# Kernel optimization log

Measured on AMD Instinct MI355X. Metric: run time of the kernel, lower is better.

Reference implementation:

```python
import jax, jax.numpy as jnp
import numpy as np

BS, GS, E, KMAX = 128, 2000, 128, 4
CLIP = 10.0
NEG = -1e30


def _gru(x, hprev, Wih, Whh, bih, bhh):
    # torch.nn.GRUCell math
    gi = x @ Wih.T + bih
    gh = hprev @ Whh.T + bhh
    ir, iz, i_n = jnp.split(gi, 3, axis=-1)
    hr, hz, h_n = jnp.split(gh, 3, axis=-1)
    r = jax.nn.sigmoid(ir + hr)
    z = jax.nn.sigmoid(iz + hz)
    n = jnp.tanh(i_n + r * h_n)
    return (1.0 - z) * n + z * hprev


def setup_inputs() -> dict:
    key = jax.random.key(0)
    it = iter(jax.random.split(key, 40))
    s = 1.0 / float(np.sqrt(E))
    u = lambda shape: jax.random.uniform(next(it), shape, jnp.float32, -s, s)
    inp = {
        "h": jax.random.normal(next(it), (BS, GS, E), jnp.float32),
        "rec": jax.random.randint(next(it), (BS, GS), 0, GS, dtype=jnp.int32),
        "context2": jax.random.normal(next(it), (BS, 9), jnp.float32),
        "visited_time": jax.random.randint(next(it), (BS, GS), 0, GS, dtype=jnp.int32),
        "last_action": jax.random.randint(next(it), (BS, 1), 0, GS, dtype=jnp.int32),
        "fixed_action": jax.random.randint(next(it), (BS, KMAX), 0, GS, dtype=jnp.int32),
    }
    for n in ["W_K1", "W_K2", "W_K3", "W_K4", "W_Q1", "W_Q2", "W_Q3", "W_Q4", "W_init"]:
        inp[n] = u((E, E))
    for n in ["b_init", "V1", "V2", "init_query"]:
        inp[n] = u((E,))
    for r in ["rnn1", "rnn2"]:
        inp[r + "_Wih"] = u((3 * E, E))
        inp[r + "_Whh"] = u((3 * E, E))
        inp[r + "_bih"] = u((3 * E,))
        inp[r + "_bhh"] = u((3 * E,))
    return inp


def _forward(h, rec, visited_time, last_action, fixed_action,
             W_K1, W_K2, W_K3, W_K4, W_Q1, W_Q2, W_Q3, W_Q4, V1, V2,
             W_init, b_init, init_query,
             rnn1_Wih, rnn1_Whh, rnn1_bih, rnn1_bhh,
             rnn2_Wih, rnn2_Whh, rnn2_bih, rnn2_bhh):
    bs, gs, e = h.shape
    cols = jnp.arange(gs)[None, :]          # [1, gs]
    rows = jnp.arange(bs)
    # K projections of h are loop-invariant: hoist them (same math as in-loop recompute)
    K1h = jnp.einsum('bge,fe->bgf', h, W_K1)
    K2h = jnp.einsum('bge,fe->bgf', h, W_K2)
    K3h = jnp.einsum('bge,fe->bgf', h, W_K3)
    K4h = jnp.einsum('bge,fe->bgf', h, W_K4)
    q1 = q2 = h.mean(1) @ W_init.T + b_init
    input_q1 = input_q2 = jnp.broadcast_to(init_query, (bs, e))
    mask = jnp.zeros((bs, gs), bool)
    stopped = jnp.ones((bs,), bool)
    nol = jnp.full((bs, 1), -1, jnp.int32)   # next_of_last_action
    ai = jnp.zeros((bs, KMAX), jnp.int32)    # action_index
    kl = jnp.zeros((bs, KMAX + 1), jnp.int32)
    kr = jnp.zeros((bs, KMAX), jnp.int32)
    ll = jnp.zeros((bs,), h.dtype)
    vtt = None
    for i in range(KMAX):
        q1 = _gru(input_q1, q1, rnn1_Wih, rnn1_Whh, rnn1_bih, rnn1_bhh)
        q2 = _gru(input_q2, q2, rnn2_Wih, rnn2_Whh, rnn2_bih, rnn2_bhh)
        s1 = (V1 * jnp.tanh(K1h + (q1 @ W_Q1.T)[:, None, :] + K3h * (q1 @ W_Q3.T)[:, None, :])).sum(-1)
        s2 = (V2 * jnp.tanh(K2h + (q2 @ W_Q2.T)[:, None, :] + K4h * (q2 @ W_Q4.T)[:, None, :])).sum(-1)
        logits = jnp.tanh(s1 + s2) * CLIP
        logits = jnp.where(mask, NEG, logits)
        if i == 0:
            logits = jnp.where(cols == last_action, NEG, logits)
        action = fixed_action[:, i:i + 1]
        if i > 0:
            action = jnp.where(stopped[:, None], ai[:, 0:1], action)
        logp = jax.nn.log_softmax(logits, axis=-1)
        loss_now = jnp.take_along_axis(logp, action, 1)[:, 0]
        ll = ll + (loss_now if i == 0 else jnp.where(stopped, 0.0, loss_now))
        nna = jnp.take_along_axis(rec, action, 1)  # next_of_new_action [bs,1]
        ai = ai.at[:, i].set(action[:, 0])
        kl = kl.at[:, i].set(jnp.where(stopped, action[:, 0], kl[:, i]))
        kr = kr.at[:, (i - 1) % KMAX].set(jnp.where(stopped, kr[:, (i - 1) % KMAX], action[:, 0]))
        kl = kl.at[:, i + 1].set(nna[:, 0])
        input_q1 = h[rows, action[:, 0]]
        input_q2 = jnp.where(stopped[:, None], input_q1, h[rows, nol[:, 0] % gs])
        eq = (action == nol)[:, 0]
        stopped = eq if i == 0 else (stopped | eq)
        kl = kl.at[:, i].set(jnp.where(stopped, kl[:, (i - 1) % (KMAX + 1)], kl[:, i]))
        kr = kr.at[:, i].set(jnp.where(stopped, kr[:, (i - 1) % KMAX], kr[:, i]))
        if i == 0:
            vtt = (visited_time - jnp.take_along_axis(visited_time, action, 1)) % gs
        vtt_a = jnp.take_along_axis(vtt, action, 1)
        mask = vtt <= vtt_a
        if i == 0:
            mask = mask | (vtt > gs - 2)
        mask = jnp.where(stopped[:, None] & (cols == action), False, mask)
        allow = (~stopped) & (nna[:, 0] == ai[:, 0])
        mask = jnp.where(allow[:, None] & (cols == ai[:, 0:1]), False, mask)
        nol = jnp.where(stopped[:, None], jnp.int32(-1), nna)
    kr = kr.at[:, KMAX - 1].set(jnp.where(~stopped, kl[:, KMAX], kr[:, KMAX - 1]))
    action_all = jnp.concatenate([ai, kl[:, :KMAX], kr], axis=-1)  # [bs, 3*KMAX]
    return action_all, ll


def reference(h, rec, context2, visited_time, last_action, fixed_action,
              W_K1, W_K2, W_K3, W_K4, W_Q1, W_Q2, W_Q3, W_Q4,
              V1, V2, W_init, b_init, init_query,
              rnn1_Wih, rnn1_Whh, rnn1_bih, rnn1_bhh,
              rnn2_Wih, rnn2_Whh, rnn2_bih, rnn2_bhh):
    # context2 unused: with_explore_stat_feature=False path (learned V1/V2)
    return _forward(h, rec, visited_time, last_action, fixed_action,
                    W_K1, W_K2, W_K3, W_K4, W_Q1, W_Q2, W_Q3, W_Q4, V1, V2,
                    W_init, b_init, init_query,
                    rnn1_Wih, rnn1_Whh, rnn1_bih, rnn1_bhh,
                    rnn2_Wih, rnn2_Whh, rnn2_bih, rnn2_bhh)
```

## Files before the change

kernel.cpp:

```cpp
#include <hip/hip_runtime.h>
#include <math.h>

#define BS 128
#define GS 2000
#define E  128
#define KMAXI 4
#define CLIPV 10.0f
#define NEGV  -1.0e30f

typedef __bf16 bf16_t;
typedef __bf16 bf16x8 __attribute__((ext_vector_type(8)));
typedef float fx4 __attribute__((ext_vector_type(4)));
typedef float fx2 __attribute__((ext_vector_type(2)));

__device__ __forceinline__ float fast_sigmoid(float x){ return 1.0f/(1.0f+__expf(-x)); }
__device__ __forceinline__ float fast_tanhf(float x){
    float e = __expf(2.0f*x);
    return 1.0f - 2.0f/(e + 1.0f);
}
__device__ __forceinline__ float pade_tanh(float x){
    float t = __builtin_amdgcn_fmed3f(x, -3.0f, 3.0f);
    float r = t*t;
    float num = t*(27.0f + r);
    float den = fmaf(9.0f, r, 27.0f);
    return num * __builtin_amdgcn_rcpf(den);
}
__device__ __forceinline__ fx2 tanh2_poly(fx2 x){
    fx2 t;
    t.x = __builtin_amdgcn_fmed3f(x.x, -3.0f, 3.0f);
    t.y = __builtin_amdgcn_fmed3f(x.y, -3.0f, 3.0f);
    fx2 r = t*t;
    fx2 q = r*(-0.0015650f) + 0.03172875f;
    q = q*r + (-0.23082094f);
    q = q*r + 0.979947f;
    return t*q;
}
__device__ __forceinline__ int pymod_s(int a){ return a < 0 ? a + GS : a; }

__device__ __forceinline__ void load_lds16(const bf16_t* g, bf16_t* l){
    __builtin_amdgcn_global_load_lds(
        (const __attribute__((address_space(1))) void*)g,
        (__attribute__((address_space(3))) void*)l, 16, 0, 0);
}

#define SC_STRIDE 64

__global__ __launch_bounds__(256) void k_hmean(
    const float* __restrict__ h, float* __restrict__ hpart,
    const int* __restrict__ rec, const int* __restrict__ vtime,
    const int* __restrict__ last_action, const int* __restrict__ fixed_action,
    int* __restrict__ sc, float* __restrict__ out)
{
    int b = blockIdx.x, p = blockIdx.y, tid = threadIdx.x;
    if (p == 16){
        if (b != 0) return;
        int t = tid;
        if (t >= BS) return;
        int stopped = 1, nol = -1;
        int ai[4]={0,0,0,0}, kl[5]={0,0,0,0,0}, kr[4]={0,0,0,0};
        int a0 = 0;
        int* scb = sc + t*SC_STRIDE;
        for (int it=0; it<KMAXI; ++it){
            int action = (it==0) ? fixed_action[t*KMAXI]
                                 : (stopped ? ai[0] : fixed_action[t*KMAXI+it]);
            int old_stopped = stopped;
            if (it==0) a0 = action;
            int vta = (it==0) ? 0 : pymod_s(vtime[(size_t)t*GS+action] - vtime[(size_t)t*GS+a0]);
            int nna = rec[(size_t)t*GS+action];
            int eq  = (action == nol) ? 1 : 0;
            int new_stopped = (it==0) ? eq : (stopped | eq);
            int ai0 = (it==0) ? action : ai[0];
            int allow = (!new_stopped) && (nna == ai0);

            ai[it] = action;
            if (old_stopped)  kl[it] = action;
            if (!old_stopped) kr[(it+3)&3] = action;
            kl[it+1] = nna;
            if (new_stopped) kl[it] = kl[(it+4)%5];
            if (new_stopped) kr[it] = kr[(it+3)&3];

            int row1 = action;
            int i2 = pymod_s(nol);
            int row2 = old_stopped ? row1 : i2;

            int* s_it = scb + 8 + it*8;
            s_it[0]=action; s_it[1]=old_stopped; s_it[2]=new_stopped;
            s_it[3]=allow;  s_it[4]=vta; s_it[5]=row1; s_it[6]=row2;

            nol = new_stopped ? -1 : nna;
            stopped = new_stopped;
        }
        scb[0] = a0;
        if (!stopped) kr[3] = kl[4];
        out[BS*12 + t] = 0.0f;
        for (int j=0;j<4;++j) out[t*12+j]   = (float)ai[j];
        for (int j=0;j<4;++j) out[t*12+4+j] = (float)kl[j];
        for (int j=0;j<4;++j) out[t*12+8+j] = (float)kr[j];
        return;
    }
    int e4 = (tid & 31) * 4;
    int gsub = tid >> 5;
    float4 acc = {0.f,0.f,0.f,0.f};
    int g0 = p*125, g1 = g0+125;
    for (int g = g0 + gsub; g < g1; g += 8){
        float4 v = *(const float4*)(h + ((size_t)b*GS + g)*E + e4);
        acc.x += v.x; acc.y += v.y; acc.z += v.z; acc.w += v.w;
    }
    __shared__ float ps[8][E];
    *(float4*)(&ps[gsub][e4]) = acc;
    __syncthreads();
    if (tid < E){
        float s = 0.f;
        #pragma unroll
        for (int j=0;j<8;++j) s += ps[j][tid];
        hpart[(b*16+p)*E + tid] = s;
    }
}

__device__ __forceinline__ float dot32(const float* a, const float* __restrict__ w){
    const float4* a4=(const float4*)a; const float4* w4=(const float4*)w;
    float s=0.f;
    #pragma unroll 8
    for (int i=0;i<32;++i){ float4 x=a4[i], y=w4[i]; s += x.x*y.x + x.y*y.y + x.z*y.z + x.w*y.w; }
    return s;
}

__global__ __launch_bounds__(384) void k_gru4(
    const float* __restrict__ hpart, const float* __restrict__ W_init,
    const float* __restrict__ b_init, const float* __restrict__ init_query,
    const float* __restrict__ h, const int* __restrict__ sc,
    const float* __restrict__ Wih1, const float* __restrict__ Whh1,
    const float* __restrict__ bih1, const float* __restrict__ bhh1,
    const float* __restrict__ Wih2, const float* __restrict__ Whh2,
    const float* __restrict__ bih2, const float* __restrict__ bhh2,
    const float* __restrict__ WQ1, const float* __restrict__ WQ2,
    const float* __restrict__ WQ3, const float* __restrict__ WQ4,
    const float* __restrict__ WK1, const float* __restrict__ WK2,
    const float* __restrict__ WK3, const float* __restrict__ WK4,
    float* __restrict__ add_buf, bf16_t* __restrict__ Mb)
{
    int b = blockIdx.x, rnn = blockIdx.y, t = threadIdx.x;
    const float* Wih = rnn ? Wih2 : Wih1;
    const float* Whh = rnn ? Whh2 : Whh1;
    const float* bih = rnn ? bih2 : bih1;
    const float* bhh = rnn ? bhh2 : bhh1;
    const float* WQa = rnn ? WQ2 : WQ1;
    const float* WQm = rnn ? WQ4 : WQ3;
    const float* WKa = rnn ? WK2 : WK1;
    const float* WKm = rnn ? WK4 : WK3;

    __shared__ float xv[E], hv[E], mv[E];
    __shared__ float gi_s[3*E], gh_s[3*E];

    if (t < E){
        float s = 0.f;
        for (int p=0;p<16;++p) s += hpart[(b*16+p)*E + t];
        xv[t] = s * (1.0f/(float)GS);
    }
    __syncthreads();
    if (t < E) hv[t] = b_init[t] + dot32(xv, W_init + (size_t)t*E);
    __syncthreads();
    if (t < E) xv[t] = init_query[t];
    __syncthreads();

    for (int s=0; s<KMAXI; ++s){
        if (s>0){
            if (t < E){
                int row = sc[b*SC_STRIDE + 8 + (s-1)*8 + (rnn==0 ? 5 : 6)];
                xv[t] = h[((size_t)b*GS + row)*E + t];
            }
            __syncthreads();
        }
        {
            float gi = bih[t] + dot32(xv, Wih + (size_t)t*E);
            float gh = bhh[t] + dot32(hv, Whh + (size_t)t*E);
            gi_s[t] = gi; gh_s[t] = gh;
        }
        __syncthreads();
        if (t < E){
            float r = fast_sigmoid(gi_s[t]     + gh_s[t]);
            float z = fast_sigmoid(gi_s[t+E]   + gh_s[t+E]);
            float n = fast_tanhf  (gi_s[t+2*E] + r*gh_s[t+2*E]);
            hv[t] = (1.f-z)*n + z*hv[t];
        }
        __syncthreads();
        int slot = s*2 + rnn;
        if (t < 2*E){
            int r = t & (E-1);
            const float* W = (t < E) ? WQa : WQm;
            float v = dot32(hv, W + (size_t)r*E);
            if (t < E) add_buf[(size_t)slot*BS*E + b*E + r] = v;
            else       mv[r] = v;
        }
        __syncthreads();
        {
            bf16x8* outp = (bf16x8*)(Mb + ((size_t)slot*BS + b)*E*E);
            for (int u = t; u < 2048; u += 384){
                int f = u >> 4, e8 = u & 15;
                int e0 = e8*8;
                float mf = mv[f];
                float4 a0 = *(const float4*)(WKa + (size_t)f*E + e0);
                float4 a1 = *(const float4*)(WKa + (size_t)f*E + e0 + 4);
                float4 m0 = *(const float4*)(WKm + (size_t)f*E + e0);
                float4 m1 = *(const float4*)(WKm + (size_t)f*E + e0 + 4);
                bf16x8 o;
                o[0]=(bf16_t)(a0.x + m0.x*mf);
                o[1]=(bf16_t)(a0.y + m0.y*mf);
                o[2]=(bf16_t)(a0.z + m0.z*mf);
                o[3]=(bf16_t)(a0.w + m0.w*mf);
                o[4]=(bf16_t)(a1.x + m1.x*mf);
                o[5]=(bf16_t)(a1.y + m1.y*mf);
                o[6]=(bf16_t)(a1.z + m1.z*mf);
                o[7]=(bf16_t)(a1.w + m1.w*mf);
                outp[f*16 + (e8 ^ (f&7))] = o;
            }
        }
        __syncthreads();
    }
}

__global__ __launch_bounds__(256) void k_scores(
    const float* __restrict__ hf, const bf16_t* __restrict__ Mb,
    const float* __restrict__ add_buf,
    const float* __restrict__ V1, const float* __restrict__ V2,
    float* __restrict__ raw4)
{
    __shared__ bf16_t sM[E*E];
    int b = blockIdx.x, yc = blockIdx.y, tid = threadIdx.x;
    int wave = tid >> 6, lane = tid & 63;
    int qd = lane >> 4, cl = lane & 15;
    int gbase = yc*256 + wave*64;

    float vv_r[2][8];
    #pragma unroll
    for (int tf=0; tf<8; ++tf){
        vv_r[0][tf] = V1[tf*16+cl];
        vv_r[1][tf] = V2[tf*16+cl];
    }

    bf16x8 afr[4][4];
    #pragma unroll
    for (int set=0; set<4; ++set){
        int grow = gbase + set*16 + cl;
        if (grow >= GS) grow = GS-1;
        const float* hrow = hf + ((size_t)b*GS + grow)*E;
        #pragma unroll
        for (int s=0;s<4;++s){
            const float* p = hrow + s*32 + qd*8;
            float4 u0 = *(const float4*)(p);
            float4 u1 = *(const float4*)(p+4);
            bf16x8 a;
            a[0]=(bf16_t)u0.x; a[1]=(bf16_t)u0.y; a[2]=(bf16_t)u0.z; a[3]=(bf16_t)u0.w;
            a[4]=(bf16_t)u1.x; a[5]=(bf16_t)u1.y; a[6]=(bf16_t)u1.z; a[7]=(bf16_t)u1.w;
            afr[set][s]=a;
        }
    }

    for (int it=0; it<KMAXI; ++it){
        fx2 acc[4][2];
        #pragma unroll
        for (int set=0;set<4;++set){ acc[set][0]=(fx2){0.f,0.f}; acc[set][1]=(fx2){0.f,0.f}; }
        #pragma unroll
        for (int arm=0; arm<2; ++arm){
            int slot = it*2 + arm;
            const bf16_t* Gm = Mb + ((size_t)slot*BS + b)*E*E;
            const float* addv = add_buf + (size_t)slot*BS*E + b*E;

            float av_r[8];
            #pragma unroll
            for (int tf=0; tf<8; ++tf) av_r[tf] = addv[tf*16+cl];

            __syncthreads();
            #pragma unroll
            for (int j=0;j<8;++j){
                int c = wave*512 + j*64 + lane;
                load_lds16(Gm + (size_t)c*8, sM + (size_t)c*8);
            }
            __syncthreads();

            #pragma unroll
            for (int tf=0; tf<8; ++tf){
                int f = tf*16 + cl;
                bf16x8 b1[4];
                #pragma unroll
                for (int s=0;s<4;++s){
                    int e8 = s*4 + qd;
                    b1[s] = *(const bf16x8*)(sM + ((size_t)(f*16 + (e8 ^ (f&7))))*8);
                }
                float av = av_r[tf];
                fx4 a0 = {av,av,av,av};
                fx4 a1 = {av,av,av,av};
                fx4 a2 = {av,av,av,av};
                fx4 a3 = {av,av,av,av};
                #pragma unroll
                for (int s=0;s<4;++s){
                    a0 = __builtin_amdgcn_mfma_f32_16x16x32_bf16(afr[0][s], b1[s], a0, 0,0,0);
                    a1 = __builtin_amdgcn_mfma_f32_16x16x32_bf16(afr[1][s], b1[s], a1, 0,0,0);
                    a2 = __builtin_amdgcn_mfma_f32_16x16x32_bf16(afr[2][s], b1[s], a2, 0,0,0);
                    a3 = __builtin_amdgcn_mfma_f32_16x16x32_bf16(afr[3][s], b1[s], a3, 0,0,0);
                }
                fx2 vv2 = {vv_r[arm][tf], vv_r[arm][tf]};
                acc[0][0] += vv2 * tanh2_poly((fx2){a0[0], a0[1]});
                acc[0][1] += vv2 * tanh2_poly((fx2){a0[2], a0[3]});
                acc[1][0] += vv2 * tanh2_poly((fx2){a1[0], a1[1]});
                acc[1][1] += vv2 * tanh2_poly((fx2){a1[2], a1[3]});
                acc[2][0] += vv2 * tanh2_poly((fx2){a2[0], a2[1]});
                acc[2][1] += vv2 * tanh2_poly((fx2){a2[2], a2[3]});
                acc[3][0] += vv2 * tanh2_poly((fx2){a3[0], a3[1]});
                acc[3][1] += vv2 * tanh2_poly((fx2){a3[2], a3[3]});
            }
        }
        #pragma unroll
        for (int set=0;set<4;++set){
            fx2 pa = acc[set][0];
            fx2 pb = acc[set][1];
            float v[4] = {pa.x, pa.y, pb.x, pb.y};
            #pragma unroll
            for (int r=0;r<4;++r){
                float s = v[r];
                s += __shfl_xor(s, 1); s += __shfl_xor(s, 2);
                s += __shfl_xor(s, 4); s += __shfl_xor(s, 8);
                v[r] = s;
            }
            if (cl==0){
                int gi = gbase + set*16 + qd*4;
                if (gi+3 < GS){
                    float4 o;
                    o.x = CLIPV*pade_tanh(v[0]);
                    o.y = CLIPV*pade_tanh(v[1]);
                    o.z = CLIPV*pade_tanh(v[2]);
                    o.w = CLIPV*pade_tanh(v[3]);
                    *(float4*)(raw4 + ((size_t)it*BS + b)*GS + gi) = o;
                }
            }
        }
    }
}

__global__ __launch_bounds__(256) void k_ll(
    const float* __restrict__ raw4, const int* __restrict__ sc,
    const int* __restrict__ vtime, const int* __restrict__ last_action,
    float* __restrict__ out)
{
    __shared__ float sL[GS];
    __shared__ float red[256];
    int b = blockIdx.x, it = blockIdx.y, t = threadIdx.x;
    const int* scb = sc + b*SC_STRIDE;
    const int* s_it = scb + 8 + it*8;
    int action = s_it[0], olds = s_it[1];
    if (it>0 && olds) return;
    int a0 = scb[0];
    int la = last_action[b];
    int vt0 = vtime[(size_t)b*GS + a0];
    int ap=0, nsp=0, alp=0, vtp=0, p = it-1;
    if (it>0){
        const int* s_p = scb + 8 + p*8;
        ap = s_p[0]; nsp = s_p[2]; alp = s_p[3]; vtp = s_p[4];
    }
    for (int g=t; g<GS; g+=256){
        float l = raw4[((size_t)it*BS + b)*GS + g];
        int m;
        if (it==0){
            m = (g==la);
        } else {
            int d = vtime[(size_t)b*GS+g] - vt0;
            if (d < 0) d += GS;
            m = (d <= vtp) ? 1 : 0;
            if (p==0 && d > GS-2) m = 1;
            if (nsp && g==ap)     m = 0;
            if (alp && g==a0)     m = 0;
        }
        sL[g] = m ? NEGV : l;
    }
    __syncthreads();
    float mx = -3.0e38f;
    for (int g=t; g<GS; g+=256) mx = fmaxf(mx, sL[g]);
    red[t]=mx; __syncthreads();
    for (int s=128;s>0;s>>=1){ if(t<s) red[t]=fmaxf(red[t],red[t+s]); __syncthreads(); }
    mx = red[0]; __syncthreads();
    float sm = 0.f;
    for (int g=t; g<GS; g+=256) sm += __expf(sL[g]-mx);
    red[t]=sm; __syncthreads();
    for (int s=128;s>0;s>>=1){ if(t<s) red[t]+=red[t+s]; __syncthreads(); }
    if (t==0){
        float lse = mx + __logf(red[0]);
        atomicAdd(&out[BS*12 + b], sL[action] - lse);
    }
}

extern "C" void kernel_launch(void* const* d_in, const int* in_sizes, int n_in,
                              void* d_out, int out_size, void* d_ws, size_t ws_size,
                              hipStream_t stream)
{
    const float* h            = (const float*)d_in[0];
    const int*   rec          = (const int*)  d_in[1];
    const int*   vtime        = (const int*)  d_in[3];
    const int*   last_action  = (const int*)  d_in[4];
    const int*   fixed_action = (const int*)  d_in[5];
    const float* WK1=(const float*)d_in[6],  *WK2=(const float*)d_in[7];
    const float* WK3=(const float*)d_in[8],  *WK4=(const float*)d_in[9];
    const float* WQ1=(const float*)d_in[10], *WQ2=(const float*)d_in[11];
    const float* WQ3=(const float*)d_in[12], *WQ4=(const float*)d_in[13];
    const float* W_init=(const float*)d_in[14];
    const float* b_init=(const float*)d_in[15];
    const float* V1=(const float*)d_in[16], *V2=(const float*)d_in[17];
    const float* init_query=(const float*)d_in[18];
    const float* Wih1=(const float*)d_in[19], *Whh1=(const float*)d_in[20];
    const float* bih1=(const float*)d_in[21], *bhh1=(const float*)d_in[22];
    const float* Wih2=(const float*)d_in[23], *Whh2=(const float*)d_in[24];
    const float* bih2=(const float*)d_in[25], *bhh2=(const float*)d_in[26];
    float* out = (float*)d_out;

    char* ws = (char*)d_ws;
    size_t off = 0;
    auto alloc = [&](size_t bytes)->char*{
        char* p = ws + off; off += (bytes + 255) & ~(size_t)255; return p;
    };
    bf16_t* Mb     = (bf16_t*)alloc((size_t)8*BS*E*E*sizeof(bf16_t));
    float*  raw4   = (float*) alloc((size_t)KMAXI*BS*GS*sizeof(float));
    float*  add_buf= (float*) alloc((size_t)8*BS*E*sizeof(float));
    float*  hpart  = (float*) alloc((size_t)BS*16*E*sizeof(float));
    int*    sc     = (int*)   alloc((size_t)BS*SC_STRIDE*sizeof(int));
    (void)in_sizes; (void)n_in; (void)out_size; (void)ws_size;

    hipLaunchKernelGGL(k_hmean, dim3(BS,17), dim3(256), 0, stream,
                       h, hpart, rec, vtime, last_action, fixed_action, sc, out);
    hipLaunchKernelGGL(k_gru4, dim3(BS,2), dim3(384), 0, stream,
                       hpart, W_init, b_init, init_query, h, sc,
                       Wih1,Whh1,bih1,bhh1, Wih2,Whh2,bih2,bhh2,
                       WQ1,WQ2,WQ3,WQ4, WK1,WK2,WK3,WK4, add_buf, Mb);
    hipLaunchKernelGGL(k_scores, dim3(BS,8), dim3(256), 0, stream,
                       h, Mb, add_buf, V1, V2, raw4);
    hipLaunchKernelGGL(k_ll, dim3(BS, KMAXI), dim3(256), 0, stream,
                       raw4, sc, vtime, last_action, out);
}
```

Measured before the change: 461.7 us.

## Halve per-block row tile in k_scores and load both arm matrices at once

The scores kernel now gives each wave 32 rows instead of 64 and launches twice as many blocks, with a launch-bounds hint of two blocks per CU. Both arm matrices for an iteration are staged into a doubled 64KB LDS buffer in one pass, which removes one barrier pair per iteration. This raises parallelism and cuts register pressure. In exchange, every block reloads the same per-batch matrices, so global and LDS traffic per output row doubles, and the larger LDS footprint may limit occupancy.

New measurement: 431.2 us. -6.6%, faster.

```diff
diff --git a/kernel.cpp b/kernel.cpp
--- a/kernel.cpp
+++ b/kernel.cpp
@@ -219,17 +219,17 @@
     }
 }
 
-__global__ __launch_bounds__(256) void k_scores(
+__global__ __launch_bounds__(256,2) void k_scores(
     const float* __restrict__ hf, const bf16_t* __restrict__ Mb,
     const float* __restrict__ add_buf,
     const float* __restrict__ V1, const float* __restrict__ V2,
     float* __restrict__ raw4)
 {
-    __shared__ bf16_t sM[E*E];
+    __shared__ bf16_t sM[2][E*E];
     int b = blockIdx.x, yc = blockIdx.y, tid = threadIdx.x;
     int wave = tid >> 6, lane = tid & 63;
     int qd = lane >> 4, cl = lane & 15;
-    int gbase = yc*256 + wave*64;
+    int gbase = yc*128 + wave*32;
 
     float vv_r[2][8];
     #pragma unroll
@@ -238,9 +238,9 @@
         vv_r[1][tf] = V2[tf*16+cl];
     }
 
-    bf16x8 afr[4][4];
+    bf16x8 afr[2][4];
     #pragma unroll
-    for (int set=0; set<4; ++set){
+    for (int set=0; set<2; ++set){
         int grow = gbase + set*16 + cl;
         if (grow >= GS) grow = GS-1;
         const float* hrow = hf + ((size_t)b*GS + grow)*E;
@@ -257,27 +257,29 @@
     }
 
     for (int it=0; it<KMAXI; ++it){
-        fx2 acc[4][2];
-        #pragma unroll
-        for (int set=0;set<4;++set){ acc[set][0]=(fx2){0.f,0.f}; acc[set][1]=(fx2){0.f,0.f}; }
+        fx2 s00={0.f,0.f}, s01={0.f,0.f}, s10={0.f,0.f}, s11={0.f,0.f};
+
+        const bf16_t* G0 = Mb + ((size_t)(it*2+0)*BS + b)*E*E;
+        const bf16_t* G1 = Mb + ((size_t)(it*2+1)*BS + b)*E*E;
+        float av_r[2][8];
+        #pragma unroll
+        for (int tf=0; tf<8; ++tf){
+            av_r[0][tf] = add_buf[(size_t)(it*2+0)*BS*E + b*E + tf*16+cl];
+            av_r[1][tf] = add_buf[(size_t)(it*2+1)*BS*E + b*E + tf*16+cl];
+        }
+
+        __syncthreads();
+        #pragma unroll
+        for (int j=0;j<8;++j){
+            int c = wave*512 + j*64 + lane;
+            load_lds16(G0 + (size_t)c*8, &sM[0][0] + (size_t)c*8);
+            load_lds16(G1 + (size_t)c*8, &sM[1][0] + (size_t)c*8);
+        }
+        __syncthreads();
+
         #pragma unroll
         for (int arm=0; arm<2; ++arm){
-            int slot = it*2 + arm;
-            const bf16_t* Gm = Mb + ((size_t)slot*BS + b)*E*E;
-            const float* addv = add_buf + (size_t)slot*BS*E + b*E;
-
-            float av_r[8];
-            #pragma unroll
-            for (int tf=0; tf<8; ++tf) av_r[tf] = addv[tf*16+cl];
-
-            __syncthreads();
-            #pragma unroll
-            for (int j=0;j<8;++j){
-                int c = wave*512 + j*64 + lane;
-                load_lds16(Gm + (size_t)c*8, sM + (size_t)c*8);
-            }
-            __syncthreads();
-
+            const bf16_t* sMc = &sM[arm][0];
             #pragma unroll
             for (int tf=0; tf<8; ++tf){
                 int f = tf*16 + cl;
@@ -285,35 +287,28 @@
                 #pragma unroll
                 for (int s=0;s<4;++s){
                     int e8 = s*4 + qd;
-                    b1[s] = *(const bf16x8*)(sM + ((size_t)(f*16 + (e8 ^ (f&7))))*8);
+                    b1[s] = *(const bf16x8*)(sMc + ((size_t)(f*16 + (e8 ^ (f&7))))*8);
                 }
-                float av = av_r[tf];
+                float av = av_r[arm][tf];
                 fx4 a0 = {av,av,av,av};
                 fx4 a1 = {av,av,av,av};
-                fx4 a2 = {av,av,av,av};
-                fx4 a3 = {av,av,av,av};
                 #pragma unroll
                 for (int s=0;s<4;++s){
                     a0 = __builtin_amdgcn_mfma_f32_16x16x32_bf16(afr[0][s], b1[s], a0, 0,0,0);
                     a1 = __builtin_amdgcn_mfma_f32_16x16x32_bf16(afr[1][s], b1[s], a1, 0,0,0);
-                    a2 = __builtin_amdgcn_mfma_f32_16x16x32_bf16(afr[2][s], b1[s], a2, 0,0,0);
-                    a3 = __builtin_amdgcn_mfma_f32_16x16x32_bf16(afr[3][s], b1[s], a3, 0,0,0);
                 }
                 fx2 vv2 = {vv_r[arm][tf], vv_r[arm][tf]};
-                acc[0][0] += vv2 * tanh2_poly((fx2){a0[0], a0[1]});
-                acc[0][1] += vv2 * tanh2_poly((fx2){a0[2], a0[3]});
-                acc[1][0] += vv2 * tanh2_poly((fx2){a1[0], a1[1]});
-                acc[1][1] += vv2 * tanh2_poly((fx2){a1[2], a1[3]});
-                acc[2][0] += vv2 * tanh2_poly((fx2){a2[0], a2[1]});
-                acc[2][1] += vv2 * tanh2_poly((fx2){a2[2], a2[3]});
-                acc[3][0] += vv2 * tanh2_poly((fx2){a3[0], a3[1]});
-                acc[3][1] += vv2 * tanh2_poly((fx2){a3[2], a3[3]});
+                s00 += vv2 * tanh2_poly((fx2){a0[0], a0[1]});
+                s01 += vv2 * tanh2_poly((fx2){a0[2], a0[3]});
+                s10 += vv2 * tanh2_poly((fx2){a1[0], a1[1]});
+                s11 += vv2 * tanh2_poly((fx2){a1[2], a1[3]});
             }
         }
-        #pragma unroll
-        for (int set=0;set<4;++set){
-            fx2 pa = acc[set][0];
-            fx2 pb = acc[set][1];
+
+        #pragma unroll
+        for (int set=0;set<2;++set){
+            fx2 pa = set ? s10 : s00;
+            fx2 pb = set ? s11 : s01;
             float v[4] = {pa.x, pa.y, pb.x, pb.y};
             #pragma unroll
             for (int r=0;r<4;++r){
@@ -429,7 +424,7 @@
                        hpart, W_init, b_init, init_query, h, sc,
                        Wih1,Whh1,bih1,bhh1, Wih2,Whh2,bih2,bhh2,
                        WQ1,WQ2,WQ3,WQ4, WK1,WK2,WK3,WK4, add_buf, Mb);
-    hipLaunchKernelGGL(k_scores, dim3(BS,8), dim3(256), 0, stream,
+    hipLaunchKernelGGL(k_scores, dim3(BS,16), dim3(256), 0, stream,
                        h, Mb, add_buf, V1, V2, raw4);
     hipLaunchKernelGGL(k_ll, dim3(BS, KMAXI), dim3(256), 0, stream,
                        raw4, sc, vtime, last_action, out);
```
